# Optimization experiments

Hardware: AMD Instinct MI355X
Metric: run time of the kernel (lower is better)

Reference implementation:

```python
import math
import jax, jax.numpy as jnp
import numpy as np

FACTOR = 5  # must match init_kwargs factor


def setup_inputs() -> dict:
    key = jax.random.key(0)
    B, L, H, D = 4, 2048, 16, 64
    k1, k2, k3, k4 = jax.random.split(key, 4)
    q = jax.random.normal(k1, (B, L, H, D), jnp.float32)
    k = jax.random.normal(k2, (B, L, H, D), jnp.float32)
    v = jax.random.normal(k3, (B, L, H, D), jnp.float32)
    sample_k = min(FACTOR * int(np.ceil(np.log(L))), L)  # = 40
    sample_idx = jax.random.randint(k4, (L, sample_k), 0, L)
    return {"q": q, "k": k, "v": v, "sample_idx": sample_idx, "attn_mask": 0}


def reference(q, k, v, sample_idx, attn_mask):
    B, L_q, H, D = q.shape
    L_k = k.shape[1]
    qh = jnp.swapaxes(q, 1, 2)  # [B,H,L_q,D]
    kh = jnp.swapaxes(k, 1, 2)  # [B,H,L_k,D]
    vh = jnp.swapaxes(v, 1, 2)  # [B,H,L_k,D]

    u_top = min(FACTOR * int(np.ceil(np.log(L_q))), L_q)

    # --- _prob_qk: sampled QK scores and sparsity measure M ---
    # k_s[b,h,q,s,d] = kh[b,h,sample_idx[q,s],d]  (per-query random key sample)
    k_s = kh[:, :, sample_idx, :]                       # [B,H,L_q,S,D]
    qk_sample = jnp.einsum('bhqd,bhqsd->bhqs', qh, k_s)  # [B,H,L_q,S]
    M = qk_sample.max(axis=-1) - qk_sample.sum(axis=-1) / L_k  # [B,H,L_q]
    _, M_top = jax.lax.top_k(M, u_top)                   # [B,H,u]

    # gather the top-u queries
    q_red = jnp.take_along_axis(qh, M_top[..., None], axis=2)  # [B,H,u,D]

    # dense scores of selected queries against all keys
    scores = jnp.einsum('bhud,bhkd->bhuk', q_red, kh) / math.sqrt(D)
    attn = jax.nn.softmax(scores, axis=-1)                     # [B,H,u,L_k]
    ctx = jnp.einsum('bhuk,bhkd->bhud', attn, vh)              # [B,H,u,D]

    # scatter context back into v at the selected query rows (RHS uses original v,
    # matching torch fancy-index assignment semantics)
    b_idx = jnp.arange(B)[:, None, None]
    h_idx = jnp.arange(H)[None, :, None]
    out = vh.at[b_idx, h_idx, M_top].set(ctx)
    return jnp.swapaxes(out, 1, 2)  # [B,L,H,D]
```

## Files before the change

### kernel.cpp

```cpp
#include <hip/hip_runtime.h>
#include <hip/hip_bf16.h>
#include <float.h>
#include <math.h>

constexpr int B = 4;
constexpr int L = 2048;
constexpr int H = 16;
constexpr int D = 64;
constexpr int U = 40;
constexpr int KROWS = 128;
constexpr int NRCH = 16;
constexpr int LPB = 16;
constexpr int CPB2 = 2048;

typedef float floatx4 __attribute__((ext_vector_type(4)));

template<int SKC>
__global__ __launch_bounds__(256) void compute_M_kernel2(const float* __restrict__ q,
                                                         const float* __restrict__ k,
                                                         const int* __restrict__ sidx,
                                                         float* __restrict__ M) {
    int blk = blockIdx.x;
    int xcd = blk & 7;
    int rest = blk >> 3;
    int bh_hi = rest & 7;
    int chunk = rest >> 3;
    int bh = bh_hi * 8 + xcd;
    int b = bh >> 4, h = bh & 15;

    int t = threadIdx.x;
    int lg = t >> 4;
    int dg = t & 15;

    __shared__ int s_idx[LPB * SKC];
    for (int i = t; i < LPB * SKC; i += 256)
        s_idx[i] = sidx[(size_t)(chunk * LPB) * SKC + i];
    __syncthreads();

    int l = chunk * LPB + lg;
    floatx4 qv = __builtin_nontemporal_load(
        reinterpret_cast<const floatx4*>(q + ((size_t)(b * L + l) * H + h) * D + dg * 4));

    float mx = -FLT_MAX;
    float sm = 0.f;
    #pragma unroll 4
    for (int s = 0; s < SKC; ++s) {
        int kidx = s_idx[lg * SKC + s];
        floatx4 kv = *reinterpret_cast<const floatx4*>(
            k + ((size_t)(b * L + kidx) * H + h) * D + dg * 4);
        float p = qv.x * kv.x + qv.y * kv.y + qv.z * kv.z + qv.w * kv.w;
        #pragma unroll
        for (int off = 8; off >= 1; off >>= 1) p += __shfl_xor(p, off, 16);
        mx = fmaxf(mx, p);
        sm += p;
    }
    if (dg == 0) {
        M[(size_t)bh * L + l] = mx - sm * (1.0f / (float)L);
    }
}

__global__ __launch_bounds__(256) void compute_M_kernel(const float* __restrict__ q,
                                                        const float* __restrict__ k,
                                                        const int* __restrict__ sidx,
                                                        float* __restrict__ M, int SK) {
    int bl = blockIdx.x;
    int b = bl / L;
    int l = bl % L;
    int t = threadIdx.x;
    int h = t >> 4;
    int dg = t & 15;

    const float* qrow = q + ((size_t)(b * L + l)) * H * D + h * D + dg * 4;
    float4 qv = *reinterpret_cast<const float4*>(qrow);

    float mx = -FLT_MAX;
    float sm = 0.f;
    for (int s = 0; s < SK; ++s) {
        int kidx = sidx[l * SK + s];
        const float* krow = k + ((size_t)(b * L + kidx)) * H * D + h * D + dg * 4;
        float4 kv = *reinterpret_cast<const float4*>(krow);
        float p = qv.x * kv.x + qv.y * kv.y + qv.z * kv.z + qv.w * kv.w;
        #pragma unroll
        for (int off = 8; off >= 1; off >>= 1) p += __shfl_xor(p, off, 16);
        mx = fmaxf(mx, p);
        sm += p;
    }
    if (dg == 0) {
        M[((size_t)(b * H + h)) * L + l] = mx - sm * (1.0f / (float)L);
    }
}

__global__ __launch_bounds__(256) void topk_copy_kernel(const float* __restrict__ M,
                                                        int* __restrict__ Mtop,
                                                        const float* __restrict__ v,
                                                        float* __restrict__ out, int n4) {
    int blk = blockIdx.x;
    int t = threadIdx.x;

    if (blk >= B * H) {
        int i = (blk - B * H) * 256 + t;
        int stride = CPB2 * 256;
        const floatx4* src = reinterpret_cast<const floatx4*>(v);
        floatx4* dst = reinterpret_cast<floatx4*>(out);
        for (; i < n4; i += stride) {
            floatx4 x = __builtin_nontemporal_load(src + i);
            __builtin_nontemporal_store(x, dst + i);
        }
        return;
    }
    if (t >= 64) return;

    int bh = blk;
    int lane = t;
    const float* m = M + (size_t)bh * L;

    float v_[32];
    #pragma unroll
    for (int j = 0; j < 32; ++j) v_[j] = m[j * 64 + lane];

    for (int u = 0; u < U; ++u) {
        float bv = -FLT_MAX;
        int bi = 0x7fffffff;
        #pragma unroll
        for (int j = 0; j < 32; ++j) {
            int idx = j * 64 + lane;
            bool take = (v_[j] > bv) || (v_[j] == bv && idx < bi);
            bv = take ? v_[j] : bv;
            bi = take ? idx : bi;
        }
        #pragma unroll
        for (int off = 1; off < 64; off <<= 1) {
            float ov = __shfl_xor(bv, off);
            int   oi = __shfl_xor(bi, off);
            bool take = (ov > bv) || (ov == bv && oi < bi);
            bv = take ? ov : bv;
            bi = take ? oi : bi;
        }
        if (lane == 0) Mtop[bh * U + u] = bi;
        #pragma unroll
        for (int j = 0; j < 32; ++j) {
            if (bi == j * 64 + lane) v_[j] = -FLT_MAX;
        }
    }
}

__global__ __launch_bounds__(256) void flash3_kernel(
        const float* __restrict__ q, const float* __restrict__ k,
        const float* __restrict__ v, const int* __restrict__ Mtop,
        float* __restrict__ pl, float* __restrict__ pacc) {
    int blk = blockIdx.x;
    int xcd = blk & 7;
    int bh = ((blk >> 3) & 7) * 8 + xcd;
    int rch = blk >> 6;
    int b = bh >> 4, h = bh & 15;
    int t = threadIdx.x;

    __shared__ __align__(16) float qs[U][D];
    __shared__ __align__(16) float lkpe[KROWS * D];
    __shared__ float redl[8][5];

    float* lk = lkpe;
    float (*pe)[KROWS] = reinterpret_cast<float (*)[KROWS]>(lkpe);

    for (int i = t; i < U * D; i += 256) {
        int u = i >> 6, dd = i & 63;
        int qi = Mtop[bh * U + u];
        qs[u][dd] = q[((size_t)(b * L + qi) * H + h) * D + dd];
    }
    {
        const floatx4* ksrc = reinterpret_cast<const floatx4*>(
            k + ((size_t)(b * L + rch * KROWS) * H + h) * D);
        floatx4* ldst = reinterpret_cast<floatx4*>(lk);
        #pragma unroll
        for (int it = 0; it < (KROWS * 16) / 256; ++it) {
            int i = it * 256 + t;
            int row = i >> 4, c = i & 15;
            ldst[i] = ksrc[(size_t)row * (H * D / 4) + c];
        }
    }
    __syncthreads();

    int rg = t & 31;
    int ug = t >> 5;
    const floatx4* lk4 = reinterpret_cast<const floatx4*>(lk);

    float s0[5], s1[5], s2[5], s3[5];
    #pragma unroll
    for (int uu = 0; uu < 5; ++uu) { s0[uu] = 0.f; s1[uu] = 0.f; s2[uu] = 0.f; s3[uu] = 0.f; }

    #pragma unroll 4
    for (int jj = 0; jj < 16; ++jj) {
        int c = (jj + rg) & 15;
        floatx4 k0 = lk4[(rg * 4 + 0) * 16 + c];
        floatx4 k1 = lk4[(rg * 4 + 1) * 16 + c];
        floatx4 k2 = lk4[(rg * 4 + 2) * 16 + c];
        floatx4 k3 = lk4[(rg * 4 + 3) * 16 + c];
        #pragma unroll
        for (int uu = 0; uu < 5; ++uu) {
            floatx4 qj = *reinterpret_cast<const floatx4*>(&qs[ug * 5 + uu][c * 4]);
            s0[uu] = fmaf(k0.x, qj.x, fmaf(k0.y, qj.y, fmaf(k0.z, qj.z, fmaf(k0.w, qj.w, s0[uu]))));
            s1[uu] = fmaf(k1.x, qj.x, fmaf(k1.y, qj.y, fmaf(k1.z, qj.z, fmaf(k1.w, qj.w, s1[uu]))));
            s2[uu] = fmaf(k2.x, qj.x, fmaf(k2.y, qj.y, fmaf(k2.z, qj.z, fmaf(k2.w, qj.w, s2[uu]))));
            s3[uu] = fmaf(k3.x, qj.x, fmaf(k3.y, qj.y, fmaf(k3.z, qj.z, fmaf(k3.w, qj.w, s3[uu]))));
        }
    }

    float e0r[5], e1r[5], e2r[5], e3r[5];
    #pragma unroll
    for (int uu = 0; uu < 5; ++uu) {
        e0r[uu] = __expf(s0[uu] * 0.125f);
        e1r[uu] = __expf(s1[uu] * 0.125f);
        e2r[uu] = __expf(s2[uu] * 0.125f);
        e3r[uu] = __expf(s3[uu] * 0.125f);
        float sv = (e0r[uu] + e1r[uu]) + (e2r[uu] + e3r[uu]);
        #pragma unroll
        for (int off = 1; off <= 16; off <<= 1) sv += __shfl_xor(sv, off);
        if ((t & 31) == 0) redl[ug][uu] = sv;
    }
    __syncthreads();

    #pragma unroll
    for (int uu = 0; uu < 5; ++uu) {
        float4 e4; e4.x = e0r[uu]; e4.y = e1r[uu]; e4.z = e2r[uu]; e4.w = e3r[uu];
        *reinterpret_cast<float4*>(&pe[ug * 5 + uu][rg * 4]) = e4;
    }
    __syncthreads();

    int d2 = t & 31;
    int ug2 = t >> 5;
    int d = d2 * 2;
    const float* vb = v + ((size_t)(b * L + rch * KROWS) * H + h) * D + d;
    float ax[5], ay[5];
    #pragma unroll
    for (int uu = 0; uu < 5; ++uu) { ax[uu] = 0.f; ay[uu] = 0.f; }
    #pragma unroll 2
    for (int row = 0; row < KROWS; row += 4) {
        float2 v0 = *reinterpret_cast<const float2*>(vb + (size_t)(row + 0) * (H * D));
        float2 v1 = *reinterpret_cast<const float2*>(vb + (size_t)(row + 1) * (H * D));
        float2 v2 = *reinterpret_cast<const float2*>(vb + (size_t)(row + 2) * (H * D));
        float2 v3 = *reinterpret_cast<const float2*>(vb + (size_t)(row + 3) * (H * D));
        #pragma unroll
        for (int uu = 0; uu < 5; ++uu) {
            float4 p4 = *reinterpret_cast<const float4*>(&pe[ug2 * 5 + uu][row]);
            ax[uu] = fmaf(p4.x, v0.x, fmaf(p4.y, v1.x, fmaf(p4.z, v2.x, fmaf(p4.w, v3.x, ax[uu]))));
            ay[uu] = fmaf(p4.x, v0.y, fmaf(p4.y, v1.y, fmaf(p4.z, v2.y, fmaf(p4.w, v3.y, ay[uu]))));
        }
    }

    size_t pb0 = (size_t)bh * U;
    #pragma unroll
    for (int uu = 0; uu < 5; ++uu) {
        int u = ug2 * 5 + uu;
        float2 o; o.x = ax[uu]; o.y = ay[uu];
        *reinterpret_cast<float2*>(&pacc[((pb0 + u) * NRCH + rch) * 64 + d]) = o;
    }
    if (t < U) {
        pl[(pb0 + t) * NRCH + rch] = redl[t / 5][t % 5];
    }
}

__global__ __launch_bounds__(256) void flash_merge_kernel(
        const float* __restrict__ pl, const float* __restrict__ pacc,
        const int* __restrict__ Mtop, float* __restrict__ out) {
    int idx = blockIdx.x * 256 + threadIdx.x;
    int dd = idx & 63;
    int bhu = idx >> 6;
    int bh = bhu / U;
    int b = bh / H, h = bh % H;

    float Lsum = 0.f;
    #pragma unroll
    for (int c = 0; c < NRCH; ++c) Lsum += pl[bhu * NRCH + c];

    float acc = 0.f;
    #pragma unroll
    for (int c = 0; c < NRCH; ++c)
        acc += pacc[((size_t)bhu * NRCH + c) * 64 + dd];

    int qi = Mtop[bhu];
    out[((size_t)(b * L + qi) * H + h) * D + dd] = acc / Lsum;
}

__global__ __launch_bounds__(256) void attn_kernel_fallback(
        const float* __restrict__ q, const float* __restrict__ k,
        const float* __restrict__ v, const int* __restrict__ Mtop,
        float* __restrict__ out) {
    int blk = blockIdx.x;
    int bh = blk / U;
    int u = blk % U;
    int b = bh / H;
    int h = bh % H;
    int qi = Mtop[bh * U + u];

    __shared__ float sc[L];
    __shared__ float qsf[D];
    __shared__ float red[4];
    __shared__ float ctx_s[4][D];

    int t = threadIdx.x;
    if (t < D) qsf[t] = q[((size_t)(b * L + qi)) * H * D + h * D + t];
    __syncthreads();

    float lm = -FLT_MAX;
    for (int i = t; i < L; i += 256) {
        const float* krow = k + ((size_t)(b * L + i)) * H * D + h * D;
        float acc = 0.f;
        #pragma unroll
        for (int dd = 0; dd < D; ++dd) acc += qsf[dd] * krow[dd];
        acc *= 0.125f;
        sc[i] = acc;
        lm = fmaxf(lm, acc);
    }
    #pragma unroll
    for (int off = 32; off >= 1; off >>= 1) lm = fmaxf(lm, __shfl_xor(lm, off));
    if ((t & 63) == 0) red[t >> 6] = lm;
    __syncthreads();
    float gm = fmaxf(fmaxf(red[0], red[1]), fmaxf(red[2], red[3]));

    float ls = 0.f;
    for (int i = t; i < L; i += 256) {
        float e = expf(sc[i] - gm);
        sc[i] = e;
        ls += e;
    }
    #pragma unroll
    for (int off = 32; off >= 1; off >>= 1) ls += __shfl_xor(ls, off);
    __syncthreads();
    if ((t & 63) == 0) red[t >> 6] = ls;
    __syncthreads();
    float inv = 1.0f / (red[0] + red[1] + red[2] + red[3]);

    int d = t & 63;
    int g = t >> 6;
    float acc = 0.f;
    for (int i = g; i < L; i += 4) {
        acc += sc[i] * v[((size_t)(b * L + i)) * H * D + h * D + d];
    }
    ctx_s[g][d] = acc;
    __syncthreads();
    if (g == 0) {
        float c = (ctx_s[0][d] + ctx_s[1][d] + ctx_s[2][d] + ctx_s[3][d]) * inv;
        out[((size_t)(b * L + qi)) * H * D + h * D + d] = c;
    }
}

extern "C" void kernel_launch(void* const* d_in, const int* in_sizes, int n_in,
                              void* d_out, int out_size, void* d_ws, size_t ws_size,
                              hipStream_t stream) {
    const float* q = (const float*)d_in[0];
    const float* k = (const float*)d_in[1];
    const float* v = (const float*)d_in[2];
    const int* sidx = (const int*)d_in[3];
    float* out = (float*)d_out;

    int SK = in_sizes[3] / L;

    size_t offM = 0;
    size_t offMtop = offM + (size_t)B * H * L * sizeof(float);
    size_t offPl = (offMtop + (size_t)B * H * U * sizeof(int) + 255) & ~(size_t)255;
    size_t offPacc = (offPl + (size_t)B * H * U * NRCH * sizeof(float) + 255) & ~(size_t)255;
    size_t needFlash = offPacc + (size_t)B * H * U * NRCH * 64 * sizeof(float);

    float* M = (float*)((char*)d_ws + offM);
    int* Mtop = (int*)((char*)d_ws + offMtop);
    float* pl = (float*)((char*)d_ws + offPl);
    float* pacc = (float*)((char*)d_ws + offPacc);

    int n4 = (B * L * H * D) / 4;

    if (SK == 40) {
        compute_M_kernel2<40><<<B * H * (L / LPB), 256, 0, stream>>>(q, k, sidx, M);
    } else {
        compute_M_kernel<<<B * L, 256, 0, stream>>>(q, k, sidx, M, SK);
    }

    topk_copy_kernel<<<B * H + CPB2, 256, 0, stream>>>(M, Mtop, v, out, n4);

    if (ws_size >= needFlash) {
        flash3_kernel<<<B * H * NRCH, 256, 0, stream>>>(q, k, v, Mtop, pl, pacc);
        flash_merge_kernel<<<B * H * U * 64 / 256, 256, 0, stream>>>(pl, pacc, Mtop, out);
    } else {
        attn_kernel_fallback<<<B * H * U, 256, 0, stream>>>(q, k, v, Mtop, out);
    }
}
```

Measured before the change: 199.2 us.

## Move v-to-out copy from top-k kernel into flash attention kernel launch

The bulk copy of v into the output now runs as extra blocks of the flash attention kernel instead of as extra blocks of the top-k kernel. Top-k becomes its own small kernel of one wave per head. The aim is to keep the serial top-k step short and overlap the bandwidth-bound copy with the compute-bound flash blocks. The risk is that copy blocks compete with flash blocks for CUs and bandwidth, and the top-k launch, which has only 64 single-wave blocks, gets no help from the copy traffic.

```diff
diff --git a/kernel.cpp b/kernel.cpp
--- a/kernel.cpp
+++ b/kernel.cpp
@@ -11,7 +11,8 @@
 constexpr int KROWS = 128;
 constexpr int NRCH = 16;
 constexpr int LPB = 16;
-constexpr int CPB2 = 2048;
+constexpr int FBLK3 = B * H * NRCH;
+constexpr int CPB3 = 1536;
 
 typedef float floatx4 __attribute__((ext_vector_type(4)));
 
@@ -90,28 +91,10 @@
     }
 }
 
-__global__ __launch_bounds__(256) void topk_copy_kernel(const float* __restrict__ M,
-                                                        int* __restrict__ Mtop,
-                                                        const float* __restrict__ v,
-                                                        float* __restrict__ out, int n4) {
-    int blk = blockIdx.x;
-    int t = threadIdx.x;
-
-    if (blk >= B * H) {
-        int i = (blk - B * H) * 256 + t;
-        int stride = CPB2 * 256;
-        const floatx4* src = reinterpret_cast<const floatx4*>(v);
-        floatx4* dst = reinterpret_cast<floatx4*>(out);
-        for (; i < n4; i += stride) {
-            floatx4 x = __builtin_nontemporal_load(src + i);
-            __builtin_nontemporal_store(x, dst + i);
-        }
-        return;
-    }
-    if (t >= 64) return;
-
-    int bh = blk;
-    int lane = t;
+__global__ __launch_bounds__(64) void topk_wave_kernel(const float* __restrict__ M,
+                                                       int* __restrict__ Mtop) {
+    int bh = blockIdx.x;
+    int lane = threadIdx.x;
     const float* m = M + (size_t)bh * L;
 
     float v_[32];
@@ -144,16 +127,30 @@
     }
 }
 
-__global__ __launch_bounds__(256) void flash3_kernel(
+__global__ __launch_bounds__(256) void flash_copy_kernel(
         const float* __restrict__ q, const float* __restrict__ k,
         const float* __restrict__ v, const int* __restrict__ Mtop,
-        float* __restrict__ pl, float* __restrict__ pacc) {
+        float* __restrict__ pl, float* __restrict__ pacc,
+        float* __restrict__ out, int n4) {
     int blk = blockIdx.x;
+    int t = threadIdx.x;
+
+    if (blk >= FBLK3) {
+        int i = (blk - FBLK3) * 256 + t;
+        int stride = CPB3 * 256;
+        const floatx4* src = reinterpret_cast<const floatx4*>(v);
+        floatx4* dst = reinterpret_cast<floatx4*>(out);
+        for (; i < n4; i += stride) {
+            floatx4 x = __builtin_nontemporal_load(src + i);
+            __builtin_nontemporal_store(x, dst + i);
+        }
+        return;
+    }
+
     int xcd = blk & 7;
     int bh = ((blk >> 3) & 7) * 8 + xcd;
     int rch = blk >> 6;
     int b = bh >> 4, h = bh & 15;
-    int t = threadIdx.x;
 
     __shared__ __align__(16) float qs[U][D];
     __shared__ __align__(16) float lkpe[KROWS * D];
@@ -279,6 +276,18 @@
 
     int qi = Mtop[bhu];
     out[((size_t)(b * L + qi) * H + h) * D + dd] = acc / Lsum;
+}
+
+__global__ __launch_bounds__(256) void copy_v_kernel(const float* __restrict__ v,
+                                                     float* __restrict__ out, int n4) {
+    int i = blockIdx.x * blockDim.x + threadIdx.x;
+    int stride = gridDim.x * blockDim.x;
+    const floatx4* src = reinterpret_cast<const floatx4*>(v);
+    floatx4* dst = reinterpret_cast<floatx4*>(out);
+    for (; i < n4; i += stride) {
+        floatx4 x = __builtin_nontemporal_load(src + i);
+        __builtin_nontemporal_store(x, dst + i);
+    }
 }
 
 __global__ __launch_bounds__(256) void attn_kernel_fallback(
@@ -367,6 +376,7 @@
     float* pacc = (float*)((char*)d_ws + offPacc);
 
     int n4 = (B * L * H * D) / 4;
+    bool flashOK = (ws_size >= needFlash);
 
     if (SK == 40) {
         compute_M_kernel2<40><<<B * H * (L / LPB), 256, 0, stream>>>(q, k, sidx, M);
@@ -374,12 +384,13 @@
         compute_M_kernel<<<B * L, 256, 0, stream>>>(q, k, sidx, M, SK);
     }
 
-    topk_copy_kernel<<<B * H + CPB2, 256, 0, stream>>>(M, Mtop, v, out, n4);
-
-    if (ws_size >= needFlash) {
-        flash3_kernel<<<B * H * NRCH, 256, 0, stream>>>(q, k, v, Mtop, pl, pacc);
+    topk_wave_kernel<<<B * H, 64, 0, stream>>>(M, Mtop);
+
+    if (flashOK) {
+        flash_copy_kernel<<<FBLK3 + CPB3, 256, 0, stream>>>(q, k, v, Mtop, pl, pacc, out, n4);
         flash_merge_kernel<<<B * H * U * 64 / 256, 256, 0, stream>>>(pl, pacc, Mtop, out);
     } else {
+        copy_v_kernel<<<2048, 256, 0, stream>>>(v, out, n4);
         attn_kernel_fallback<<<B * H * U, 256, 0, stream>>>(q, k, v, Mtop, out);
     }
 }
```

Result: no change. 201.8 us (+1.3%).
